# Kernel tuning notes

Measured on AMD Instinct MI355X. Metric: run time of the kernel, lower is better.

The kernel has to match this reference:

```python
import jax, jax.numpy as jnp
import numpy as np

N = 50000      # nodes
E = 800000     # edges
IN = 64        # in_feats
HID = 4        # hidden_size
OUT = 64       # out_feats
COORS = 3
EPS = 1e-07
NEG_SLOPE = 0.01  # F.leaky_relu default


def setup_inputs() -> dict:
    key = jax.random.key(0)
    ks = jax.random.split(key, 10)
    feat = jax.random.normal(ks[0], (N, IN), dtype=jnp.float32)
    pos = jax.random.normal(ks[1], (N, COORS), dtype=jnp.float32)
    src = jax.random.randint(ks[2], (E,), 0, N, dtype=jnp.int32)
    dst = jax.random.randint(ks[3], (E,), 0, N, dtype=jnp.int32)
    W_self = jax.random.normal(ks[4], (OUT, IN), dtype=jnp.float32) * 0.1
    W_sp = jax.random.normal(ks[5], (HID * IN, COORS), dtype=jnp.float32) * 0.3
    b_sp = jax.random.normal(ks[6], (HID * IN,), dtype=jnp.float32) * 0.05
    W_neigh = jax.random.normal(ks[7], (OUT, HID * IN), dtype=jnp.float32) * 0.05
    b_neigh = jax.random.normal(ks[8], (OUT,), dtype=jnp.float32) * 0.05
    bias = jnp.zeros((OUT,), dtype=jnp.float32)
    return {"feat": feat, "pos": pos, "src": src, "dst": dst,
            "W_self": W_self, "W_sp": W_sp, "b_sp": b_sp,
            "W_neigh": W_neigh, "b_neigh": b_neigh, "bias": bias}


def reference(feat, pos, src, dst, W_self, W_sp, b_sp, W_neigh, b_neigh, bias):
    # per-edge spatial weighting
    rel = pos[dst] - pos[src]                                   # [E, 3]
    scal = jnp.linalg.norm(rel, axis=1, keepdims=True) + EPS    # [E, 1]
    ws = (rel + 1.0) / scal                                     # [E, 3]
    s = jax.nn.leaky_relu(ws @ W_sp.T + b_sp, NEG_SLOPE)        # [E, HID*IN]
    # modulate gathered src features: reshape(E, IN, HID) * h_src[:, :, None]
    msg = (s.reshape(E, IN, HID) * feat[src][:, :, None]).reshape(E, IN * HID)
    # mean aggregation per destination node (zero for isolated nodes)
    neigh_sum = jax.ops.segment_sum(msg, dst, num_segments=N)   # [N, IN*HID]
    cnt = jax.ops.segment_sum(jnp.ones((E,), feat.dtype), dst, num_segments=N)
    neigh_h = neigh_sum / jnp.maximum(cnt, 1.0)[:, None]
    # output projections
    h_neigh = neigh_h @ W_neigh.T + b_neigh                     # [N, OUT]
    rst = feat @ W_self.T + h_neigh + bias                      # [N, OUT]
    return rst
```

## Files before the change

kernel.cpp:

```cpp
#include <hip/hip_runtime.h>
#include <math.h>

#define N_NODES 50000
#define N_EDGES 800000
#define EPS 1e-7f
#define NEG_SLOPE 0.01f

#define BUCKET 64
#define GSTRIDE 72
#define EDGE_BLOCKS (N_EDGES / 256)
#define FEAT_BLOCKS (N_NODES * 64 / 4 / 256)

typedef __attribute__((ext_vector_type(8))) short short8;
typedef __attribute__((ext_vector_type(4))) float f32x4;

__device__ __forceinline__ unsigned bf16_rne(float x) {
    unsigned u = __float_as_uint(x);
    u += 0x7fffu + ((u >> 16) & 1u);
    return u >> 16;
}
__device__ __forceinline__ unsigned pack_bf16(float a, float b) {
    return bf16_rne(a) | (bf16_rne(b) << 16);
}


__global__ __launch_bounds__(256) void prep_kernel(
    const int* __restrict__ src, const int* __restrict__ dst,
    const float* __restrict__ pos, const float* __restrict__ feat,
    int* __restrict__ cnt, uint2* __restrict__ gdata,
    uint2* __restrict__ featb2,
    const float* __restrict__ W_neigh, const float* __restrict__ W_self,
    const float* __restrict__ b_neigh, const float* __restrict__ bias,
    unsigned* __restrict__ wnp, unsigned* __restrict__ wsp, float* __restrict__ bb)
{
    const int bid = blockIdx.x;

    if (bid < EDGE_BLOCKS) {
        const int i = bid * 256 + threadIdx.x;
        const int s = src[i], d = dst[i];
        const float sx = pos[s * 3 + 0], sy = pos[s * 3 + 1], sz = pos[s * 3 + 2];
        const float dx = pos[d * 3 + 0], dy = pos[d * 3 + 1], dz = pos[d * 3 + 2];
        const float rx = dx - sx, ry = dy - sy, rz = dz - sz;
        const float inv =
            __builtin_amdgcn_rcpf(__builtin_amdgcn_sqrtf(rx * rx + ry * ry + rz * rz) + EPS);
        const uint2 rec = make_uint2(pack_bf16((rx + 1.f) * inv, (ry + 1.f) * inv),
                                     bf16_rne((rz + 1.f) * inv) | ((unsigned)s << 16));
        const int p = atomicAdd(&cnt[d], 1);
        if (p < BUCKET) gdata[(size_t)d * GSTRIDE + p] = rec;
        return;
    }

    if (bid == EDGE_BLOCKS) {
        const int t = threadIdx.x;
        const float2* Wn2 = (const float2*)W_neigh;
        const float2* Ws2 = (const float2*)W_self;
        for (int i = t; i < 64 * 128; i += 256) {
            float2 v = Wn2[i];
            wnp[i] = pack_bf16(v.x, v.y);
        }
        for (int i = t; i < 64 * 32; i += 256) {
            float2 v = Ws2[i];
            wsp[i] = pack_bf16(v.x, v.y);
        }
        if (t < 64) bb[t] = b_neigh[t] + bias[t];
        return;
    }

    const int idx = (bid - EDGE_BLOCKS - 1) * 256 + threadIdx.x;
    float4 v = reinterpret_cast<const float4*>(feat)[idx];
    featb2[idx] = make_uint2(pack_bf16(v.x, v.y), pack_bf16(v.z, v.w));
}


#define ACC_STRIDE 264

__device__ __forceinline__ float featload(const unsigned short* featb, unsigned rec_y, int lane) {
    return __uint_as_float((unsigned)featb[(size_t)(rec_y >> 16) * 64 + lane] << 16);
}

__global__ __launch_bounds__(256) void aggregate_project_kernel(
    const unsigned short* __restrict__ featb, const float* __restrict__ W_sp,
    const float* __restrict__ b_sp, const int* __restrict__ cnt,
    const uint2* __restrict__ gdata, const short* __restrict__ wnb,
    const short* __restrict__ wsb, const float* __restrict__ bb,
    float* __restrict__ out)
{
    __shared__ unsigned short accS[16 * ACC_STRIDE];

    const int lane = threadIdx.x & 63;
    const int w = threadIdx.x >> 6;
    const int nb = blockIdx.x << 4;

    float wsp0[4], wsp1[4], wsp2[4], bsp[4];
#pragma unroll
    for (int h = 0; h < 4; ++h) {
        int j = lane * 4 + h;
        wsp0[h] = W_sp[j * 3 + 0];
        wsp1[h] = W_sp[j * 3 + 1];
        wsp2[h] = W_sp[j * 3 + 2];
        bsp[h]  = b_sp[j];
    }

#define MLP_ACC(U, F)                                                              \
    {                                                                              \
        const float wx = __uint_as_float((U).x << 16);                             \
        const float wy = __uint_as_float((U).x & 0xffff0000u);                     \
        const float wz = __uint_as_float((U).y << 16);                             \
        float t0 = fmaf(wx, wsp0[0], fmaf(wy, wsp1[0], fmaf(wz, wsp2[0], bsp[0])));\
        float t1 = fmaf(wx, wsp0[1], fmaf(wy, wsp1[1], fmaf(wz, wsp2[1], bsp[1])));\
        float t2 = fmaf(wx, wsp0[2], fmaf(wy, wsp1[2], fmaf(wz, wsp2[2], bsp[2])));\
        float t3 = fmaf(wx, wsp0[3], fmaf(wy, wsp1[3], fmaf(wz, wsp2[3], bsp[3])));\
        a0 = fmaf(fmaxf(t0, t0 * NEG_SLOPE), (F), a0);                             \
        a1 = fmaf(fmaxf(t1, t1 * NEG_SLOPE), (F), a1);                             \
        a2 = fmaf(fmaxf(t2, t2 * NEG_SLOPE), (F), a2);                             \
        a3 = fmaf(fmaxf(t3, t3 * NEG_SLOPE), (F), a3);                             \
    }

    for (int q = 0; q < 4; ++q) {
        const int r = (w << 2) + q;
        const int n = nb + r;
        const int degt = __builtin_amdgcn_readfirstlane(cnt[n]);
        const int deg = min(degt, BUCKET);
        const uint2* gp = gdata + (size_t)n * GSTRIDE;

        float a0 = 0.f, a1 = 0.f, a2 = 0.f, a3 = 0.f;

        if (deg > 0) {
            const int dm = deg - 1;
            uint2 u0 = gp[0];
            uint2 u1 = gp[1];
            uint2 u2 = gp[2];
            uint2 u3 = gp[3];
            uint2 u4 = gp[4];
            uint2 u5 = gp[5];
            float f0 = featload(featb, u0.y, lane);
            float f1 = featload(featb, u1.y, lane);
            float f2 = featload(featb, u2.y, lane);
            float f3 = featload(featb, u3.y, lane);

            for (int e = 0; e < deg; e += 2) {
                uint2 u6 = gp[e + 6];
                uint2 u7 = gp[e + 7];
                float f4 = featload(featb, u4.y, lane);
                float f5 = featload(featb, u5.y, lane);

                MLP_ACC(u0, f0)
                {
                    const float fm = (e + 1 <= dm) ? f1 : 0.f;
                    MLP_ACC(u1, fm)
                }

                u0 = u2; u1 = u3; u2 = u4; u3 = u5; u4 = u6; u5 = u7;
                f0 = f2; f1 = f3; f2 = f4; f3 = f5;
            }
        }

        const float mscale = 1.f / fmaxf((float)degt, 1.f);
        uint2 pv = make_uint2(pack_bf16(a0 * mscale, a1 * mscale),
                              pack_bf16(a2 * mscale, a3 * mscale));
        *reinterpret_cast<uint2*>(&accS[r * ACC_STRIDE + lane * 4]) = pv;
    }
#undef MLP_ACC
    __syncthreads();

    const int mrow = lane & 15;
    const int quad = lane >> 4;
    const int o = (w << 4) + mrow;

    f32x4 acc = {0.f, 0.f, 0.f, 0.f};

    const unsigned short* Ar = &accS[mrow * ACC_STRIDE + quad * 8];
    const short* Br = wnb + o * 256 + quad * 8;
#pragma unroll
    for (int ks = 0; ks < 8; ++ks) {
        short8 a = *reinterpret_cast<const short8*>(Ar + ks * 32);
        short8 b = *reinterpret_cast<const short8*>(Br + ks * 32);
        acc = __builtin_amdgcn_mfma_f32_16x16x32_bf16(a, b, acc, 0, 0, 0);
    }

    const short* Fr = (const short*)featb + (size_t)(nb + mrow) * 64 + quad * 8;
    const short* Sr = wsb + o * 64 + quad * 8;
#pragma unroll
    for (int ks = 0; ks < 2; ++ks) {
        short8 a = *reinterpret_cast<const short8*>(Fr + ks * 32);
        short8 b = *reinterpret_cast<const short8*>(Sr + ks * 32);
        acc = __builtin_amdgcn_mfma_f32_16x16x32_bf16(a, b, acc, 0, 0, 0);
    }

    const float badd = bb[o];
#pragma unroll
    for (int r = 0; r < 4; ++r) {
        out[(size_t)(nb + quad * 4 + r) * 64 + o] = acc[r] + badd;
    }
}


extern "C" void kernel_launch(void* const* d_in, const int* in_sizes, int n_in,
                              void* d_out, int out_size, void* d_ws, size_t ws_size,
                              hipStream_t stream) {
    (void)in_sizes; (void)n_in; (void)out_size; (void)ws_size;
    const float* feat    = (const float*)d_in[0];
    const float* pos     = (const float*)d_in[1];
    const int*   src     = (const int*)d_in[2];
    const int*   dst     = (const int*)d_in[3];
    const float* W_self  = (const float*)d_in[4];
    const float* W_sp    = (const float*)d_in[5];
    const float* b_sp    = (const float*)d_in[6];
    const float* W_neigh = (const float*)d_in[7];
    const float* b_neigh = (const float*)d_in[8];
    const float* bias    = (const float*)d_in[9];
    float* out = (float*)d_out;

    uint2*        gdata  = (uint2*)d_ws;
    uint2*        featb2 = gdata + (size_t)N_NODES * GSTRIDE;
    unsigned int* wnp    = (unsigned int*)(featb2 + 800000);
    unsigned int* wsp    = wnp + 8192;
    float*        bb     = (float*)(wsp + 2048);
    int*          cnt    = (int*)(bb + 64);

    hipMemsetAsync(cnt, 0, (size_t)N_NODES * sizeof(int), stream);
    prep_kernel<<<EDGE_BLOCKS + 1 + FEAT_BLOCKS, 256, 0, stream>>>(
        src, dst, pos, feat, cnt, gdata, featb2,
        W_neigh, W_self, b_neigh, bias, wnp, wsp, bb);
    aggregate_project_kernel<<<N_NODES / 16, 256, 0, stream>>>(
        (const unsigned short*)featb2, W_sp, b_sp, cnt, gdata,
        (const short*)wnp, (const short*)wsp, bb, out);
}
```

Measured before the change: 191.9 us.

## Stage edge records in LDS and split prep into separate kernels

The aggregate kernel now bulk-loads each block's 16 nodes' edge-record buckets into shared memory with one coalesced copy, then reads records from LDS. With record loads now cheap, the software pipeline in the inner loop is shortened from 6-ahead to 2-ahead. The fused prep kernel is split into a feature-packing kernel and an edge histogram/geometry kernel launched back to back. This trades scattered global loads for a full-bucket copy, which includes unused slots for low-degree nodes, an extra barrier, more LDS per block, and one extra launch.

Result: faster. 185.6 us (-3.3%).

```diff
diff --git a/kernel.cpp b/kernel.cpp
--- a/kernel.cpp
+++ b/kernel.cpp
@@ -24,33 +24,33 @@
 }
 
 
-__global__ __launch_bounds__(256) void prep_kernel(
+__global__ __launch_bounds__(256) void hist_geom_kernel(
     const int* __restrict__ src, const int* __restrict__ dst,
-    const float* __restrict__ pos, const float* __restrict__ feat,
-    int* __restrict__ cnt, uint2* __restrict__ gdata,
-    uint2* __restrict__ featb2,
+    const float* __restrict__ pos, int* __restrict__ cnt,
+    uint2* __restrict__ gdata)
+{
+    const int i = blockIdx.x * 256 + threadIdx.x;
+    const int s = src[i], d = dst[i];
+    const float sx = pos[s * 3 + 0], sy = pos[s * 3 + 1], sz = pos[s * 3 + 2];
+    const float dx = pos[d * 3 + 0], dy = pos[d * 3 + 1], dz = pos[d * 3 + 2];
+    const float rx = dx - sx, ry = dy - sy, rz = dz - sz;
+    const float inv =
+        __builtin_amdgcn_rcpf(__builtin_amdgcn_sqrtf(rx * rx + ry * ry + rz * rz) + EPS);
+    const uint2 rec = make_uint2(pack_bf16((rx + 1.f) * inv, (ry + 1.f) * inv),
+                                 bf16_rne((rz + 1.f) * inv) | ((unsigned)s << 16));
+    const int p = atomicAdd(&cnt[d], 1);
+    if (p < BUCKET) gdata[(size_t)d * GSTRIDE + p] = rec;
+}
+
+
+__global__ __launch_bounds__(256) void featpack_kernel(
+    const float* __restrict__ feat, uint2* __restrict__ featb2,
     const float* __restrict__ W_neigh, const float* __restrict__ W_self,
     const float* __restrict__ b_neigh, const float* __restrict__ bias,
     unsigned* __restrict__ wnp, unsigned* __restrict__ wsp, float* __restrict__ bb)
 {
     const int bid = blockIdx.x;
-
-    if (bid < EDGE_BLOCKS) {
-        const int i = bid * 256 + threadIdx.x;
-        const int s = src[i], d = dst[i];
-        const float sx = pos[s * 3 + 0], sy = pos[s * 3 + 1], sz = pos[s * 3 + 2];
-        const float dx = pos[d * 3 + 0], dy = pos[d * 3 + 1], dz = pos[d * 3 + 2];
-        const float rx = dx - sx, ry = dy - sy, rz = dz - sz;
-        const float inv =
-            __builtin_amdgcn_rcpf(__builtin_amdgcn_sqrtf(rx * rx + ry * ry + rz * rz) + EPS);
-        const uint2 rec = make_uint2(pack_bf16((rx + 1.f) * inv, (ry + 1.f) * inv),
-                                     bf16_rne((rz + 1.f) * inv) | ((unsigned)s << 16));
-        const int p = atomicAdd(&cnt[d], 1);
-        if (p < BUCKET) gdata[(size_t)d * GSTRIDE + p] = rec;
-        return;
-    }
-
-    if (bid == EDGE_BLOCKS) {
+    if (bid == FEAT_BLOCKS) {
         const int t = threadIdx.x;
         const float2* Wn2 = (const float2*)W_neigh;
         const float2* Ws2 = (const float2*)W_self;
@@ -65,8 +65,7 @@
         if (t < 64) bb[t] = b_neigh[t] + bias[t];
         return;
     }
-
-    const int idx = (bid - EDGE_BLOCKS - 1) * 256 + threadIdx.x;
+    const int idx = bid * 256 + threadIdx.x;
     float4 v = reinterpret_cast<const float4*>(feat)[idx];
     featb2[idx] = make_uint2(pack_bf16(v.x, v.y), pack_bf16(v.z, v.w));
 }
@@ -86,10 +85,16 @@
     float* __restrict__ out)
 {
     __shared__ unsigned short accS[16 * ACC_STRIDE];
+    __shared__ uint2 recS[16 * GSTRIDE];
 
     const int lane = threadIdx.x & 63;
     const int w = threadIdx.x >> 6;
     const int nb = blockIdx.x << 4;
+
+    {
+        const uint2* gsrc = gdata + (size_t)nb * GSTRIDE;
+        for (int i = threadIdx.x; i < 16 * GSTRIDE; i += 256) recS[i] = gsrc[i];
+    }
 
     float wsp0[4], wsp1[4], wsp2[4], bsp[4];
 #pragma unroll
@@ -100,6 +105,7 @@
         wsp2[h] = W_sp[j * 3 + 2];
         bsp[h]  = b_sp[j];
     }
+    __syncthreads();
 
 #define MLP_ACC(U, F)                                                              \
     {                                                                              \
@@ -121,7 +127,7 @@
         const int n = nb + r;
         const int degt = __builtin_amdgcn_readfirstlane(cnt[n]);
         const int deg = min(degt, BUCKET);
-        const uint2* gp = gdata + (size_t)n * GSTRIDE;
+        const uint2* gp = &recS[r * GSTRIDE];
 
         float a0 = 0.f, a1 = 0.f, a2 = 0.f, a3 = 0.f;
 
@@ -129,20 +135,14 @@
             const int dm = deg - 1;
             uint2 u0 = gp[0];
             uint2 u1 = gp[1];
-            uint2 u2 = gp[2];
-            uint2 u3 = gp[3];
-            uint2 u4 = gp[4];
-            uint2 u5 = gp[5];
             float f0 = featload(featb, u0.y, lane);
             float f1 = featload(featb, u1.y, lane);
-            float f2 = featload(featb, u2.y, lane);
-            float f3 = featload(featb, u3.y, lane);
 
             for (int e = 0; e < deg; e += 2) {
-                uint2 u6 = gp[e + 6];
-                uint2 u7 = gp[e + 7];
-                float f4 = featload(featb, u4.y, lane);
-                float f5 = featload(featb, u5.y, lane);
+                uint2 u2 = gp[e + 2];
+                uint2 u3 = gp[e + 3];
+                float f2 = featload(featb, u2.y, lane);
+                float f3 = featload(featb, u3.y, lane);
 
                 MLP_ACC(u0, f0)
                 {
@@ -150,8 +150,8 @@
                     MLP_ACC(u1, fm)
                 }
 
-                u0 = u2; u1 = u3; u2 = u4; u3 = u5; u4 = u6; u5 = u7;
-                f0 = f2; f1 = f3; f2 = f4; f3 = f5;
+                u0 = u2; u1 = u3;
+                f0 = f2; f1 = f3;
             }
         }
 
@@ -219,9 +219,9 @@
     int*          cnt    = (int*)(bb + 64);
 
     hipMemsetAsync(cnt, 0, (size_t)N_NODES * sizeof(int), stream);
-    prep_kernel<<<EDGE_BLOCKS + 1 + FEAT_BLOCKS, 256, 0, stream>>>(
-        src, dst, pos, feat, cnt, gdata, featb2,
-        W_neigh, W_self, b_neigh, bias, wnp, wsp, bb);
+    featpack_kernel<<<FEAT_BLOCKS + 1, 256, 0, stream>>>(
+        feat, featb2, W_neigh, W_self, b_neigh, bias, wnp, wsp, bb);
+    hist_geom_kernel<<<EDGE_BLOCKS, 256, 0, stream>>>(src, dst, pos, cnt, gdata);
     aggregate_project_kernel<<<N_NODES / 16, 256, 0, stream>>>(
         (const unsigned short*)featb2, W_sp, b_sp, cnt, gdata,
         (const short*)wnp, (const short*)wsp, bb, out);
```

## Stage edge records in LDS and use packed f32x2 math for the edge MLP

Applied to the files above, without the earlier changes.

Each wave now loads the bucketed edge records for its four destination nodes into shared memory with one coalesced load per row, instead of reading them serially from global memory inside the edge loop. The bucket stride shrinks from 72 to 66, which reduces the padding that is allocated and read. The per-edge spatial MLP and leaky-ReLU accumulation are rewritten with 2-wide float vectors so the compiler can emit packed FMA instructions, and the software prefetch depth for records and features drops from six to two. The shallower prefetch leaves less latency hiding for the gathered feature loads. Slots 64 and 65 of the LDS rows are never written, and the loop can read them as lookahead records when a node has close to 64 edges.

Result: no change. 189.6 us (-1.2%).

```diff
diff --git a/kernel.cpp b/kernel.cpp
--- a/kernel.cpp
+++ b/kernel.cpp
@@ -7,12 +7,13 @@
 #define NEG_SLOPE 0.01f
 
 #define BUCKET 64
-#define GSTRIDE 72
+#define GSTRIDE 66
 #define EDGE_BLOCKS (N_EDGES / 256)
 #define FEAT_BLOCKS (N_NODES * 64 / 4 / 256)
 
 typedef __attribute__((ext_vector_type(8))) short short8;
 typedef __attribute__((ext_vector_type(4))) float f32x4;
+typedef __attribute__((ext_vector_type(2))) float f32x2;
 
 __device__ __forceinline__ unsigned bf16_rne(float x) {
     unsigned u = __float_as_uint(x);
@@ -27,8 +28,7 @@
 __global__ __launch_bounds__(256) void prep_kernel(
     const int* __restrict__ src, const int* __restrict__ dst,
     const float* __restrict__ pos, const float* __restrict__ feat,
-    int* __restrict__ cnt, uint2* __restrict__ gdata,
-    uint2* __restrict__ featb2,
+    int* __restrict__ cnt, uint2* __restrict__ gdata, uint2* __restrict__ featb2,
     const float* __restrict__ W_neigh, const float* __restrict__ W_self,
     const float* __restrict__ b_neigh, const float* __restrict__ bias,
     unsigned* __restrict__ wnp, unsigned* __restrict__ wsp, float* __restrict__ bb)
@@ -86,34 +86,45 @@
     float* __restrict__ out)
 {
     __shared__ unsigned short accS[16 * ACC_STRIDE];
+    __shared__ uint2 recS[16 * GSTRIDE];
 
     const int lane = threadIdx.x & 63;
     const int w = threadIdx.x >> 6;
     const int nb = blockIdx.x << 4;
 
-    float wsp0[4], wsp1[4], wsp2[4], bsp[4];
-#pragma unroll
-    for (int h = 0; h < 4; ++h) {
-        int j = lane * 4 + h;
-        wsp0[h] = W_sp[j * 3 + 0];
-        wsp1[h] = W_sp[j * 3 + 1];
-        wsp2[h] = W_sp[j * 3 + 2];
-        bsp[h]  = b_sp[j];
-    }
-
-#define MLP_ACC(U, F)                                                              \
-    {                                                                              \
-        const float wx = __uint_as_float((U).x << 16);                             \
-        const float wy = __uint_as_float((U).x & 0xffff0000u);                     \
-        const float wz = __uint_as_float((U).y << 16);                             \
-        float t0 = fmaf(wx, wsp0[0], fmaf(wy, wsp1[0], fmaf(wz, wsp2[0], bsp[0])));\
-        float t1 = fmaf(wx, wsp0[1], fmaf(wy, wsp1[1], fmaf(wz, wsp2[1], bsp[1])));\
-        float t2 = fmaf(wx, wsp0[2], fmaf(wy, wsp1[2], fmaf(wz, wsp2[2], bsp[2])));\
-        float t3 = fmaf(wx, wsp0[3], fmaf(wy, wsp1[3], fmaf(wz, wsp2[3], bsp[3])));\
-        a0 = fmaf(fmaxf(t0, t0 * NEG_SLOPE), (F), a0);                             \
-        a1 = fmaf(fmaxf(t1, t1 * NEG_SLOPE), (F), a1);                             \
-        a2 = fmaf(fmaxf(t2, t2 * NEG_SLOPE), (F), a2);                             \
-        a3 = fmaf(fmaxf(t3, t3 * NEG_SLOPE), (F), a3);                             \
+#pragma unroll
+    for (int q = 0; q < 4; ++q) {
+        const int r = (w << 2) + q;
+        recS[r * GSTRIDE + lane] = gdata[(size_t)(nb + r) * GSTRIDE + lane];
+    }
+
+    f32x2 w0A, w0B, w1A, w1B, w2A, w2B, bA, bB;
+    {
+        const int j = lane * 4;
+        w0A = (f32x2){W_sp[(j + 0) * 3 + 0], W_sp[(j + 1) * 3 + 0]};
+        w0B = (f32x2){W_sp[(j + 2) * 3 + 0], W_sp[(j + 3) * 3 + 0]};
+        w1A = (f32x2){W_sp[(j + 0) * 3 + 1], W_sp[(j + 1) * 3 + 1]};
+        w1B = (f32x2){W_sp[(j + 2) * 3 + 1], W_sp[(j + 3) * 3 + 1]};
+        w2A = (f32x2){W_sp[(j + 0) * 3 + 2], W_sp[(j + 1) * 3 + 2]};
+        w2B = (f32x2){W_sp[(j + 2) * 3 + 2], W_sp[(j + 3) * 3 + 2]};
+        bA  = (f32x2){b_sp[j + 0], b_sp[j + 1]};
+        bB  = (f32x2){b_sp[j + 2], b_sp[j + 3]};
+    }
+    const f32x2 slope2 = {NEG_SLOPE, NEG_SLOPE};
+
+#define MLP_ACC(U, F)                                                  \
+    {                                                                  \
+        const float wx = __uint_as_float((U).x << 16);                 \
+        const float wy = __uint_as_float((U).x & 0xffff0000u);         \
+        const float wz = __uint_as_float((U).y << 16);                 \
+        const f32x2 wx2 = {wx, wx}, wy2 = {wy, wy}, wz2 = {wz, wz};    \
+        const f32x2 F2 = {(F), (F)};                                   \
+        f32x2 tA = wx2 * w0A + wy2 * w1A + wz2 * w2A + bA;             \
+        f32x2 tB = wx2 * w0B + wy2 * w1B + wz2 * w2B + bB;             \
+        tA = __builtin_elementwise_max(tA, tA * slope2);               \
+        tB = __builtin_elementwise_max(tB, tB * slope2);               \
+        aA += tA * F2;                                                 \
+        aB += tB * F2;                                                 \
     }
 
     for (int q = 0; q < 4; ++q) {
@@ -121,28 +132,22 @@
         const int n = nb + r;
         const int degt = __builtin_amdgcn_readfirstlane(cnt[n]);
         const int deg = min(degt, BUCKET);
-        const uint2* gp = gdata + (size_t)n * GSTRIDE;
-
-        float a0 = 0.f, a1 = 0.f, a2 = 0.f, a3 = 0.f;
+        const uint2* gp = &recS[r * GSTRIDE];
+
+        f32x2 aA = {0.f, 0.f}, aB = {0.f, 0.f};
 
         if (deg > 0) {
             const int dm = deg - 1;
             uint2 u0 = gp[0];
             uint2 u1 = gp[1];
-            uint2 u2 = gp[2];
-            uint2 u3 = gp[3];
-            uint2 u4 = gp[4];
-            uint2 u5 = gp[5];
             float f0 = featload(featb, u0.y, lane);
             float f1 = featload(featb, u1.y, lane);
-            float f2 = featload(featb, u2.y, lane);
-            float f3 = featload(featb, u3.y, lane);
 
             for (int e = 0; e < deg; e += 2) {
-                uint2 u6 = gp[e + 6];
-                uint2 u7 = gp[e + 7];
-                float f4 = featload(featb, u4.y, lane);
-                float f5 = featload(featb, u5.y, lane);
+                uint2 u2 = gp[e + 2];
+                uint2 u3 = gp[e + 3];
+                float f2 = featload(featb, u2.y, lane);
+                float f3 = featload(featb, u3.y, lane);
 
                 MLP_ACC(u0, f0)
                 {
@@ -150,14 +155,14 @@
                     MLP_ACC(u1, fm)
                 }
 
-                u0 = u2; u1 = u3; u2 = u4; u3 = u5; u4 = u6; u5 = u7;
-                f0 = f2; f1 = f3; f2 = f4; f3 = f5;
+                u0 = u2; u1 = u3;
+                f0 = f2; f1 = f3;
             }
         }
 
         const float mscale = 1.f / fmaxf((float)degt, 1.f);
-        uint2 pv = make_uint2(pack_bf16(a0 * mscale, a1 * mscale),
-                              pack_bf16(a2 * mscale, a3 * mscale));
+        uint2 pv = make_uint2(pack_bf16(aA.x * mscale, aA.y * mscale),
+                              pack_bf16(aB.x * mscale, aB.y * mscale));
         *reinterpret_cast<uint2*>(&accS[r * ACC_STRIDE + lane * 4]) = pv;
     }
 #undef MLP_ACC
```
